# Kernel tuning notes

Hardware: AMD Instinct MI355X
Metric: run time of the kernel (lower is better)

## Reference

```python
import jax, jax.numpy as jnp
import numpy as np

N = 100000      # nodes (H3 lattice cells)
E = 600000      # directed edges (avg degree ~6, hexagonal)
D_IN, D_H, D_E = 256, 128, 64


def _init_linear(key, fan_in, fan_out):
    kw, kb = jax.random.split(key)
    s = 1.0 / np.sqrt(fan_in)
    W = jax.random.uniform(kw, (fan_in, fan_out), jnp.float32, -s, s)
    b = jax.random.uniform(kb, (fan_out,), jnp.float32, -s, s)
    return W, b


def setup_inputs() -> dict:
    key = jax.random.key(0)
    ks = jax.random.split(key, 8)
    W1, b1 = _init_linear(ks[2], D_IN, D_H)
    W2, b2 = _init_linear(ks[3], D_H, D_H)
    W3, b3 = _init_linear(ks[4], D_H, D_E)
    Wd1, bd1 = _init_linear(ks[5], D_E, D_H)
    Wd2, bd2 = _init_linear(ks[6], D_H, D_IN)
    return {
        "x": jax.random.normal(ks[0], (N, D_IN), jnp.float32),
        "edge_index": jax.random.randint(ks[1], (2, E), 0, N, dtype=jnp.int64),
        "W1": W1, "b1": b1, "W2": W2, "b2": b2, "W3": W3, "b3": b3,
        "Wd1": Wd1, "bd1": bd1, "Wd2": Wd2, "bd2": bd2,
    }


def _gcn_conv(x, src, dst, W, b):
    """PyG GCNConv: add self-loops, sym deg^{-1/2} norm, linear, scatter-add, bias."""
    n = x.shape[0]
    h = x @ W                                                  # [N, out]
    ones = jnp.ones(src.shape[0], x.dtype)
    deg = jax.ops.segment_sum(ones, dst, num_segments=n) + 1.0  # +1 for self-loop
    dinv = jax.lax.rsqrt(deg)                                   # deg >= 1 always
    coef = dinv[src] * dinv[dst]                                # [E]
    agg = jax.ops.segment_sum(h[src] * coef[:, None], dst, num_segments=n)
    agg = agg + h * (dinv * dinv)[:, None]                      # self-loop term
    return agg + b


def reference(x, edge_index, W1, b1, W2, b2, W3, b3, Wd1, bd1, Wd2, bd2):
    src, dst = edge_index[0], edge_index[1]
    # Encoder (dropout is identity in eval mode)
    h = jax.nn.relu(_gcn_conv(x, src, dst, W1, b1))
    h = jax.nn.relu(_gcn_conv(h, src, dst, W2, b2))
    z = _gcn_conv(h, src, dst, W3, b3)                          # [N, D_E]
    # Decoder
    x_hat = jax.nn.relu(z @ Wd1 + bd1) @ Wd2 + bd2              # [N, D_IN]
    return (z, x_hat)
```

## Files before the change

kernel.cpp:

```cpp
#include <hip/hip_runtime.h>

#define DIN 256
#define DH  128
#define DE  64


__global__ void init_counts_kernel(int* __restrict__ counts, int n) {
    int i = blockIdx.x * blockDim.x + threadIdx.x;
    if (i < n) counts[i] = 0;
}

__global__ void count_edges_kernel(const int* __restrict__ dst,
                                   int* __restrict__ counts, int E) {
    int e = blockIdx.x * blockDim.x + threadIdx.x;
    if (e < E) atomicAdd(&counts[dst[e]], 1);
}

__global__ void dinv_kernel(const int* __restrict__ counts,
                            float* __restrict__ dinv, int n) {
    int i = blockIdx.x * blockDim.x + threadIdx.x;
    if (i < n) dinv[i] = rsqrtf((float)counts[i] + 1.0f);
}

__global__ void scan1_kernel(const int* __restrict__ counts,
                             int* __restrict__ rowptr,
                             int* __restrict__ blocksums, int n) {
    __shared__ int sd[256];
    int t = threadIdx.x;
    int base = blockIdx.x * 1024 + t * 4;
    int v[4];
#pragma unroll
    for (int i = 0; i < 4; i++) v[i] = (base + i < n) ? counts[base + i] : 0;
    int tsum = v[0] + v[1] + v[2] + v[3];
    sd[t] = tsum;
    __syncthreads();
    for (int off = 1; off < 256; off <<= 1) {
        int x = (t >= off) ? sd[t - off] : 0;
        __syncthreads();
        sd[t] += x;
        __syncthreads();
    }
    int p = sd[t] - tsum;
#pragma unroll
    for (int i = 0; i < 4; i++) {
        if (base + i < n) rowptr[base + i] = p;
        p += v[i];
    }
    if (t == 255) blocksums[blockIdx.x] = sd[255];
}

__global__ void scan2_kernel(int* __restrict__ blocksums, int nb) {
    if (threadIdx.x == 0 && blockIdx.x == 0) {
        int run = 0;
        for (int i = 0; i < nb; i++) {
            int x = blocksums[i];
            blocksums[i] = run;
            run += x;
        }
    }
}

__global__ void scan3_kernel(int* __restrict__ rowptr, int* __restrict__ cursor,
                             const int* __restrict__ blocksums, int n, int E) {
    int i = blockIdx.x * blockDim.x + threadIdx.x;
    if (i < n) {
        int r = rowptr[i] + blocksums[i >> 10];
        rowptr[i] = r;
        cursor[i] = r;
    }
    if (i == 0) rowptr[n] = E;
}

__global__ void fill_csr_kernel(const int* __restrict__ src,
                                const int* __restrict__ dst,
                                const float* __restrict__ dinv,
                                int* __restrict__ cursor,
                                int* __restrict__ csr_src,
                                float* __restrict__ csr_coef, int E) {
    int e = blockIdx.x * blockDim.x + threadIdx.x;
    if (e >= E) return;
    int s = src[e], d = dst[e];
    int pos = atomicAdd(&cursor[d], 1);
    csr_src[pos] = s;
    csr_coef[pos] = dinv[s] * dinv[d];
}


__global__ __launch_bounds__(256) void gemm_kernel(
    const float* __restrict__ A, const float* __restrict__ W,
    const float* __restrict__ bias, float* __restrict__ C,
    int M, int K, int N, int relu) {
    __shared__ float As[32][132];
    __shared__ float Bs[32][68];
    int tid = threadIdx.x;
    int tx = tid & 15;
    int ty = tid >> 4;
    int row0 = blockIdx.x * 128, col0 = blockIdx.y * 64;

    float acc[8][4] = {};

    int a_kq = (tid & 7) * 4;
    int a_r  = tid >> 3;
    int b_c  = (tid & 15) * 4;
    int b_kr = tid >> 4;

    for (int k0 = 0; k0 < K; k0 += 32) {
#pragma unroll
        for (int i = 0; i < 4; i++) {
            int r = a_r + i * 32;
            int gr = row0 + r;
            float4 v = make_float4(0.f, 0.f, 0.f, 0.f);
            if (gr < M) v = *(const float4*)&A[(size_t)gr * K + k0 + a_kq];
            As[a_kq + 0][r] = v.x;
            As[a_kq + 1][r] = v.y;
            As[a_kq + 2][r] = v.z;
            As[a_kq + 3][r] = v.w;
        }
#pragma unroll
        for (int i = 0; i < 2; i++) {
            int kr = b_kr + i * 16;
            *(float4*)&Bs[kr][b_c] =
                *(const float4*)&W[(size_t)(k0 + kr) * N + col0 + b_c];
        }
        __syncthreads();

#pragma unroll 8
        for (int kk = 0; kk < 32; kk++) {
            float4 a0 = *(const float4*)&As[kk][ty * 8];
            float4 a1 = *(const float4*)&As[kk][ty * 8 + 4];
            float4 b  = *(const float4*)&Bs[kk][tx * 4];
            float am[8] = {a0.x, a0.y, a0.z, a0.w, a1.x, a1.y, a1.z, a1.w};
#pragma unroll
            for (int i = 0; i < 8; i++) {
                acc[i][0] = fmaf(am[i], b.x, acc[i][0]);
                acc[i][1] = fmaf(am[i], b.y, acc[i][1]);
                acc[i][2] = fmaf(am[i], b.z, acc[i][2]);
                acc[i][3] = fmaf(am[i], b.w, acc[i][3]);
            }
        }
        __syncthreads();
    }

    float4 bv = make_float4(0.f, 0.f, 0.f, 0.f);
    if (bias) bv = *(const float4*)&bias[col0 + tx * 4];
#pragma unroll
    for (int i = 0; i < 8; i++) {
        int r = row0 + ty * 8 + i;
        if (r >= M) continue;
        float4 c;
        c.x = acc[i][0] + bv.x;
        c.y = acc[i][1] + bv.y;
        c.z = acc[i][2] + bv.z;
        c.w = acc[i][3] + bv.w;
        if (relu) {
            c.x = fmaxf(c.x, 0.f);
            c.y = fmaxf(c.y, 0.f);
            c.z = fmaxf(c.z, 0.f);
            c.w = fmaxf(c.w, 0.f);
        }
        *(float4*)&C[(size_t)r * N + col0 + tx * 4] = c;
    }
}


template <int D, bool RELU>
__global__ __launch_bounds__(256) void agg_kernel(
    const float* __restrict__ h, const float* __restrict__ dinv,
    const int* __restrict__ rowptr, const int* __restrict__ csr_src,
    const float* __restrict__ csr_coef, const float* __restrict__ bias,
    float* __restrict__ out, int n) {
    constexpr int TPN = D / 4;
    constexpr int NPB = 256 / TPN;
    int v = blockIdx.x * NPB + threadIdx.x / TPN;
    int d4 = (threadIdx.x % TPN) * 4;
    if (v >= n) return;

    float di = dinv[v];
    float s2 = di * di;
    float4 hv = *(const float4*)&h[(size_t)v * D + d4];
    float4 bv = *(const float4*)&bias[d4];
    float4 acc0, acc1;
    acc0.x = fmaf(hv.x, s2, bv.x);
    acc0.y = fmaf(hv.y, s2, bv.y);
    acc0.z = fmaf(hv.z, s2, bv.z);
    acc0.w = fmaf(hv.w, s2, bv.w);
    acc1 = make_float4(0.f, 0.f, 0.f, 0.f);

    int e0 = rowptr[v], e1 = rowptr[v + 1];
    int e = e0;
    for (; e + 2 <= e1; e += 2) {
        int s0 = csr_src[e];
        int s1 = csr_src[e + 1];
        float c0 = csr_coef[e];
        float c1 = csr_coef[e + 1];
        float4 g0 = *(const float4*)&h[(size_t)s0 * D + d4];
        float4 g1 = *(const float4*)&h[(size_t)s1 * D + d4];
        acc0.x = fmaf(g0.x, c0, acc0.x);
        acc0.y = fmaf(g0.y, c0, acc0.y);
        acc0.z = fmaf(g0.z, c0, acc0.z);
        acc0.w = fmaf(g0.w, c0, acc0.w);
        acc1.x = fmaf(g1.x, c1, acc1.x);
        acc1.y = fmaf(g1.y, c1, acc1.y);
        acc1.z = fmaf(g1.z, c1, acc1.z);
        acc1.w = fmaf(g1.w, c1, acc1.w);
    }
    if (e < e1) {
        int s0 = csr_src[e];
        float c0 = csr_coef[e];
        float4 g0 = *(const float4*)&h[(size_t)s0 * D + d4];
        acc0.x = fmaf(g0.x, c0, acc0.x);
        acc0.y = fmaf(g0.y, c0, acc0.y);
        acc0.z = fmaf(g0.z, c0, acc0.z);
        acc0.w = fmaf(g0.w, c0, acc0.w);
    }
    float4 r;
    r.x = acc0.x + acc1.x;
    r.y = acc0.y + acc1.y;
    r.z = acc0.z + acc1.z;
    r.w = acc0.w + acc1.w;
    if (RELU) {
        r.x = fmaxf(r.x, 0.f);
        r.y = fmaxf(r.y, 0.f);
        r.z = fmaxf(r.z, 0.f);
        r.w = fmaxf(r.w, 0.f);
    }
    *(float4*)&out[(size_t)v * D + d4] = r;
}


extern "C" void kernel_launch(void* const* d_in, const int* in_sizes, int n_in,
                              void* d_out, int out_size, void* d_ws,
                              size_t ws_size, hipStream_t stream) {
    const float* x   = (const float*)d_in[0];
    const int*   ei  = (const int*)d_in[1];
    const float* W1  = (const float*)d_in[2];
    const float* b1  = (const float*)d_in[3];
    const float* W2  = (const float*)d_in[4];
    const float* b2  = (const float*)d_in[5];
    const float* W3  = (const float*)d_in[6];
    const float* b3  = (const float*)d_in[7];
    const float* Wd1 = (const float*)d_in[8];
    const float* bd1 = (const float*)d_in[9];
    const float* Wd2 = (const float*)d_in[10];
    const float* bd2 = (const float*)d_in[11];

    const int N = in_sizes[0] / DIN;
    const int E = in_sizes[1] / 2;
    const int* src = ei;
    const int* dst = ei + E;

    char* w = (char*)d_ws;
    auto alloc = [&](size_t bytes) -> char* {
        char* p = w;
        w += (bytes + 255) & ~(size_t)255;
        return p;
    };
    int*   counts    = (int*)alloc((size_t)N * 4);
    float* dinv      = (float*)alloc((size_t)N * 4);
    int*   rowptr    = (int*)alloc((size_t)(N + 1) * 4);
    int*   cursor    = (int*)alloc((size_t)N * 4);
    int*   blocksums = (int*)alloc(4096);
    int*   csr_src   = (int*)alloc((size_t)E * 4);
    float* csr_coef  = (float*)alloc((size_t)E * 4);
    float* Abuf      = (float*)alloc((size_t)N * DH * 4);

    float* zout = (float*)d_out;
    float* xhat = zout + (size_t)N * DE;
    float* S1   = xhat;

    dim3 blk(256);
    int gN = (N + 255) / 256, gE = (E + 255) / 256;

    init_counts_kernel<<<gN, blk, 0, stream>>>(counts, N);
    count_edges_kernel<<<gE, blk, 0, stream>>>(dst, counts, E);
    dinv_kernel<<<gN, blk, 0, stream>>>(counts, dinv, N);
    int nb = (N + 1023) / 1024;
    scan1_kernel<<<nb, blk, 0, stream>>>(counts, rowptr, blocksums, N);
    scan2_kernel<<<1, 64, 0, stream>>>(blocksums, nb);
    scan3_kernel<<<gN, blk, 0, stream>>>(rowptr, cursor, blocksums, N, E);
    fill_csr_kernel<<<gE, blk, 0, stream>>>(src, dst, dinv, cursor, csr_src,
                                            csr_coef, E);

    int mt = (N + 127) / 128;

    gemm_kernel<<<dim3(mt, DH / 64), blk, 0, stream>>>(x, W1, nullptr, S1, N,
                                                       DIN, DH, 0);
    agg_kernel<DH, true><<<dim3((N + 7) / 8), blk, 0, stream>>>(
        S1, dinv, rowptr, csr_src, csr_coef, b1, Abuf, N);
    gemm_kernel<<<dim3(mt, DH / 64), blk, 0, stream>>>(Abuf, W2, nullptr, S1, N,
                                                       DH, DH, 0);
    agg_kernel<DH, true><<<dim3((N + 7) / 8), blk, 0, stream>>>(
        S1, dinv, rowptr, csr_src, csr_coef, b2, Abuf, N);
    gemm_kernel<<<dim3(mt, DE / 64), blk, 0, stream>>>(Abuf, W3, nullptr, S1, N,
                                                       DH, DE, 0);
    agg_kernel<DE, false><<<dim3((N + 15) / 16), blk, 0, stream>>>(
        S1, dinv, rowptr, csr_src, csr_coef, b3, zout, N);
    gemm_kernel<<<dim3(mt, DH / 64), blk, 0, stream>>>(zout, Wd1, bd1, Abuf, N,
                                                       DE, DH, 1);
    gemm_kernel<<<dim3(mt, DIN / 64), blk, 0, stream>>>(Abuf, Wd2, bd2, xhat, N,
                                                        DH, DIN, 0);
}
```

Baseline: 691.8 us.

## Replace FP32 SIMT GEMMs with split-bf16 MFMA GEMMs

Swaps the shared-memory tiled FP32 FMA GEMM for a matrix-core kernel that splits each FP32 operand into a high and a low bf16 part. It accumulates three bf16 MFMA products (hi*hi, lo*hi, hi*lo) per step to keep accuracy close to FP32. Weights are pre-split and transposed by a small kernel on every call, while activations are split in registers. The aim is to move GEMM throughput onto matrix cores. The costs are extra conversion ALU work, A loads straight from global memory with no LDS reuse, and scalar (non-vectorized) output stores.

```diff
diff --git a/kernel.cpp b/kernel.cpp
--- a/kernel.cpp
+++ b/kernel.cpp
@@ -3,6 +3,17 @@
 #define DIN 256
 #define DH  128
 #define DE  64
+
+typedef __attribute__((ext_vector_type(8))) short short8;
+typedef __attribute__((ext_vector_type(4))) float f32x4;
+
+__device__ inline unsigned short f2bf(float f) {
+    unsigned u = __float_as_uint(f);
+    return (unsigned short)((u + 0x7FFFu + ((u >> 16) & 1u)) >> 16);
+}
+__device__ inline float bf2f(unsigned short h) {
+    return __uint_as_float((unsigned)h << 16);
+}
 
 
 __global__ void init_counts_kernel(int* __restrict__ counts, int n) {
@@ -86,79 +97,76 @@
 }
 
 
-__global__ __launch_bounds__(256) void gemm_kernel(
-    const float* __restrict__ A, const float* __restrict__ W,
-    const float* __restrict__ bias, float* __restrict__ C,
-    int M, int K, int N, int relu) {
-    __shared__ float As[32][132];
-    __shared__ float Bs[32][68];
+__global__ void wsplit_kernel(const float* __restrict__ W,
+                              unsigned short* __restrict__ Wh,
+                              unsigned short* __restrict__ Wl, int K, int N) {
+    int i = blockIdx.x * blockDim.x + threadIdx.x;
+    if (i >= K * N) return;
+    int k = i / N, n = i % N;
+    float v = W[i];
+    unsigned short h = f2bf(v);
+    Wh[(size_t)n * K + k] = h;
+    Wl[(size_t)n * K + k] = f2bf(v - bf2f(h));
+}
+
+
+template <int K, int NF, bool RELU, bool BIAS>
+__global__ __launch_bounds__(256) void mfma_gemm(
+    const float* __restrict__ A, const unsigned short* __restrict__ Wh,
+    const unsigned short* __restrict__ Wl, const float* __restrict__ bias,
+    float* __restrict__ C, int M) {
+    constexpr int N = NF * 16;
     int tid = threadIdx.x;
-    int tx = tid & 15;
-    int ty = tid >> 4;
-    int row0 = blockIdx.x * 128, col0 = blockIdx.y * 64;
-
-    float acc[8][4] = {};
-
-    int a_kq = (tid & 7) * 4;
-    int a_r  = tid >> 3;
-    int b_c  = (tid & 15) * 4;
-    int b_kr = tid >> 4;
+    int wid = tid >> 6;
+    int l = tid & 63;
+    int lr = l & 15, lk = l >> 4;
+    int row0 = (blockIdx.x * 4 + wid) * 16;
+    int arow = row0 + lr;
+    const float* ap = A + (size_t)(arow < M ? arow : 0) * K + lk * 8;
+    const unsigned short* bhp = Wh + (size_t)lr * K + lk * 8;
+    const unsigned short* blp = Wl + (size_t)lr * K + lk * 8;
+
+    f32x4 acc[NF];
+#pragma unroll
+    for (int j = 0; j < NF; j++) acc[j] = (f32x4){0.f, 0.f, 0.f, 0.f};
 
     for (int k0 = 0; k0 < K; k0 += 32) {
-#pragma unroll
-        for (int i = 0; i < 4; i++) {
-            int r = a_r + i * 32;
-            int gr = row0 + r;
-            float4 v = make_float4(0.f, 0.f, 0.f, 0.f);
-            if (gr < M) v = *(const float4*)&A[(size_t)gr * K + k0 + a_kq];
-            As[a_kq + 0][r] = v.x;
-            As[a_kq + 1][r] = v.y;
-            As[a_kq + 2][r] = v.z;
-            As[a_kq + 3][r] = v.w;
+        float4 a0 = *(const float4*)(ap + k0);
+        float4 a1 = *(const float4*)(ap + k0 + 4);
+        float av[8] = {a0.x, a0.y, a0.z, a0.w, a1.x, a1.y, a1.z, a1.w};
+        short8 ah, al;
+#pragma unroll
+        for (int e = 0; e < 8; e++) {
+            unsigned short h = f2bf(av[e]);
+            ah[e] = (short)h;
+            al[e] = (short)f2bf(av[e] - bf2f(h));
         }
 #pragma unroll
-        for (int i = 0; i < 2; i++) {
-            int kr = b_kr + i * 16;
-            *(float4*)&Bs[kr][b_c] =
-                *(const float4*)&W[(size_t)(k0 + kr) * N + col0 + b_c];
+        for (int j = 0; j < NF; j++) {
+            short8 bh = *(const short8*)(bhp + (size_t)j * 16 * K + k0);
+            short8 bl = *(const short8*)(blp + (size_t)j * 16 * K + k0);
+            acc[j] = __builtin_amdgcn_mfma_f32_16x16x32_bf16(ah, bh, acc[j],
+                                                             0, 0, 0);
+            acc[j] = __builtin_amdgcn_mfma_f32_16x16x32_bf16(al, bh, acc[j],
+                                                             0, 0, 0);
+            acc[j] = __builtin_amdgcn_mfma_f32_16x16x32_bf16(ah, bl, acc[j],
+                                                             0, 0, 0);
         }
-        __syncthreads();
-
-#pragma unroll 8
-        for (int kk = 0; kk < 32; kk++) {
-            float4 a0 = *(const float4*)&As[kk][ty * 8];
-            float4 a1 = *(const float4*)&As[kk][ty * 8 + 4];
-            float4 b  = *(const float4*)&Bs[kk][tx * 4];
-            float am[8] = {a0.x, a0.y, a0.z, a0.w, a1.x, a1.y, a1.z, a1.w};
-#pragma unroll
-            for (int i = 0; i < 8; i++) {
-                acc[i][0] = fmaf(am[i], b.x, acc[i][0]);
-                acc[i][1] = fmaf(am[i], b.y, acc[i][1]);
-                acc[i][2] = fmaf(am[i], b.z, acc[i][2]);
-                acc[i][3] = fmaf(am[i], b.w, acc[i][3]);
+    }
+
+#pragma unroll
+    for (int j = 0; j < NF; j++) {
+        int col = j * 16 + lr;
+        float bb = BIAS ? bias[col] : 0.f;
+#pragma unroll
+        for (int e = 0; e < 4; e++) {
+            int r = row0 + lk * 4 + e;
+            if (r < M) {
+                float v = acc[j][e] + bb;
+                if (RELU) v = fmaxf(v, 0.f);
+                C[(size_t)r * N + col] = v;
             }
         }
-        __syncthreads();
-    }
-
-    float4 bv = make_float4(0.f, 0.f, 0.f, 0.f);
-    if (bias) bv = *(const float4*)&bias[col0 + tx * 4];
-#pragma unroll
-    for (int i = 0; i < 8; i++) {
-        int r = row0 + ty * 8 + i;
-        if (r >= M) continue;
-        float4 c;
-        c.x = acc[i][0] + bv.x;
-        c.y = acc[i][1] + bv.y;
-        c.z = acc[i][2] + bv.z;
-        c.w = acc[i][3] + bv.w;
-        if (relu) {
-            c.x = fmaxf(c.x, 0.f);
-            c.y = fmaxf(c.y, 0.f);
-            c.z = fmaxf(c.z, 0.f);
-            c.w = fmaxf(c.w, 0.f);
-        }
-        *(float4*)&C[(size_t)r * N + col0 + tx * 4] = c;
     }
 }
 
@@ -263,6 +271,16 @@
     int*   csr_src   = (int*)alloc((size_t)E * 4);
     float* csr_coef  = (float*)alloc((size_t)E * 4);
     float* Abuf      = (float*)alloc((size_t)N * DH * 4);
+    unsigned short* W1h  = (unsigned short*)alloc(DIN * DH * 2);
+    unsigned short* W1l  = (unsigned short*)alloc(DIN * DH * 2);
+    unsigned short* W2h  = (unsigned short*)alloc(DH * DH * 2);
+    unsigned short* W2l  = (unsigned short*)alloc(DH * DH * 2);
+    unsigned short* W3h  = (unsigned short*)alloc(DH * DE * 2);
+    unsigned short* W3l  = (unsigned short*)alloc(DH * DE * 2);
+    unsigned short* Wd1h = (unsigned short*)alloc(DE * DH * 2);
+    unsigned short* Wd1l = (unsigned short*)alloc(DE * DH * 2);
+    unsigned short* Wd2h = (unsigned short*)alloc(DH * DIN * 2);
+    unsigned short* Wd2l = (unsigned short*)alloc(DH * DIN * 2);
 
     float* zout = (float*)d_out;
     float* xhat = zout + (size_t)N * DE;
@@ -281,22 +299,33 @@
     fill_csr_kernel<<<gE, blk, 0, stream>>>(src, dst, dinv, cursor, csr_src,
                                             csr_coef, E);
 
-    int mt = (N + 127) / 128;
-
-    gemm_kernel<<<dim3(mt, DH / 64), blk, 0, stream>>>(x, W1, nullptr, S1, N,
-                                                       DIN, DH, 0);
+    wsplit_kernel<<<(DIN * DH + 255) / 256, blk, 0, stream>>>(W1, W1h, W1l,
+                                                              DIN, DH);
+    wsplit_kernel<<<(DH * DH + 255) / 256, blk, 0, stream>>>(W2, W2h, W2l,
+                                                             DH, DH);
+    wsplit_kernel<<<(DH * DE + 255) / 256, blk, 0, stream>>>(W3, W3h, W3l,
+                                                             DH, DE);
+    wsplit_kernel<<<(DE * DH + 255) / 256, blk, 0, stream>>>(Wd1, Wd1h, Wd1l,
+                                                             DE, DH);
+    wsplit_kernel<<<(DH * DIN + 255) / 256, blk, 0, stream>>>(Wd2, Wd2h, Wd2l,
+                                                              DH, DIN);
+
+    int gg = (N + 63) / 64;
+
+    mfma_gemm<DIN, DH / 16, false, false><<<gg, blk, 0, stream>>>(
+        x, W1h, W1l, nullptr, S1, N);
     agg_kernel<DH, true><<<dim3((N + 7) / 8), blk, 0, stream>>>(
         S1, dinv, rowptr, csr_src, csr_coef, b1, Abuf, N);
-    gemm_kernel<<<dim3(mt, DH / 64), blk, 0, stream>>>(Abuf, W2, nullptr, S1, N,
-                                                       DH, DH, 0);
+    mfma_gemm<DH, DH / 16, false, false><<<gg, blk, 0, stream>>>(
+        Abuf, W2h, W2l, nullptr, S1, N);
     agg_kernel<DH, true><<<dim3((N + 7) / 8), blk, 0, stream>>>(
         S1, dinv, rowptr, csr_src, csr_coef, b2, Abuf, N);
-    gemm_kernel<<<dim3(mt, DE / 64), blk, 0, stream>>>(Abuf, W3, nullptr, S1, N,
-                                                       DH, DE, 0);
+    mfma_gemm<DH, DE / 16, false, false><<<gg, blk, 0, stream>>>(
+        Abuf, W3h, W3l, nullptr, S1, N);
     agg_kernel<DE, false><<<dim3((N + 15) / 16), blk, 0, stream>>>(
         S1, dinv, rowptr, csr_src, csr_coef, b3, zout, N);
-    gemm_kernel<<<dim3(mt, DH / 64), blk, 0, stream>>>(zout, Wd1, bd1, Abuf, N,
-                                                       DE, DH, 1);
-    gemm_kernel<<<dim3(mt, DIN / 64), blk, 0, stream>>>(Abuf, Wd2, bd2, xhat, N,
-                                                        DH, DIN, 0);
-}
+    mfma_gemm<DE, DH / 16, true, true><<<gg, blk, 0, stream>>>(
+        zout, Wd1h, Wd1l, bd1, Abuf, N);
+    mfma_gemm<DH, DIN / 16, false, true><<<gg, blk, 0, stream>>>(
+        Abuf, Wd2h, Wd2l, bd2, xhat, N);
+}
```

Result: slower. 820.2 us (+18.5%).
